# Performance work log

Hardware: AMD Instinct MI355X
Metric: run time of the kernel (lower is better)

Reference implementation:

```python
import jax, jax.numpy as jnp
import numpy as np

SCORE_T = 0.4   # self.score_t
NMS_T = 0.4     # self.nms_t
TOP_K = 200     # nms top_k


def setup_inputs() -> dict:
    key = jax.random.key(0)
    k1, k2, k3, k4, k5 = jax.random.split(key, 5)
    B, S, A, C = 1, 32768, 8, 80
    return {
        "box_pred": jax.random.normal(k1, (B, S, A, 4), jnp.float32),
        "box_conf": jax.random.uniform(k2, (B, S, A, 1), jnp.float32),
        "box_prob": jax.random.uniform(k3, (B, S, A, C), jnp.float32),
        "priors": jax.random.uniform(k4, (B, S, A, 4), jnp.float32),
        "img_shape": jax.random.uniform(k5, (1, 4), jnp.float32),
    }


def _decode(box_pred, box_conf, box_prob, priors, img_shape):
    # box decode: xy += prior xy, wh *= prior wh; then corners
    xy = box_pred[..., 0:2] + priors[..., 0:2]
    wh = box_pred[..., 2:4] * priors[..., 2:4]
    corners = jnp.concatenate([xy - 0.5 * wh, xy + 0.5 * wh], axis=-1)
    # grid normalization: x by 30, y by 10
    corners = corners / jnp.asarray([30.0, 10.0, 30.0, 10.0], corners.dtype)
    # class scores = objectness * class prob, max over classes
    all_scores = box_conf * box_prob                     # [B,S,A,C]
    cls_scores = jnp.max(all_scores, axis=-1)            # [B,S,A]
    cls_ids = jnp.argmax(all_scores, axis=-1)            # [B,S,A]
    valid = cls_scores > SCORE_T
    # flatten candidates; scale to image coords (same math as scaling post-filter)
    boxes = corners.reshape(-1, 4) * img_shape.reshape(1, 4)
    scores = jnp.where(valid.reshape(-1), cls_scores.reshape(-1), -1.0)
    classes = cls_ids.reshape(-1).astype(jnp.int32)
    return boxes, scores, classes


def _greedy_nms_keep(top_boxes, top_scores):
    # padded greedy NMS over the fixed top-K candidates (score-desc order)
    valid = top_scores > SCORE_T  # padded/invalid entries carry score -1
    b = jax.lax.stop_gradient(top_boxes)
    x1, y1, x2, y2 = b[:, 0], b[:, 1], b[:, 2], b[:, 3]
    area = (x2 - x1) * (y2 - y1)
    xx1 = jnp.maximum(x1[:, None], x1[None, :])
    yy1 = jnp.maximum(y1[:, None], y1[None, :])
    xx2 = jnp.minimum(x2[:, None], x2[None, :])
    yy2 = jnp.minimum(y2[:, None], y2[None, :])
    inter = jnp.clip(xx2 - xx1, 0.0) * jnp.clip(yy2 - yy1, 0.0)
    iou = inter / (area[:, None] + area[None, :] - inter)  # [K,K]
    idxs = jnp.arange(TOP_K)

    def body(i, keep):
        # candidate i (highest remaining score), suppress later overlapping boxes
        sup = keep[i] & (iou[i] > NMS_T) & (idxs > i)
        return keep & ~sup

    return jax.lax.fori_loop(0, TOP_K, body, valid)


def reference(box_pred, box_conf, box_prob, priors, img_shape):
    boxes, scores, classes = _decode(box_pred, box_conf, box_prob, priors, img_shape)
    top_scores, top_idx = jax.lax.top_k(scores, TOP_K)
    top_boxes = boxes[top_idx]
    top_classes = classes[top_idx]
    keep = _greedy_nms_keep(top_boxes, top_scores)
    count = jnp.sum(keep).astype(jnp.int32)
    # compact kept detections to the front (score-descending), zero-pad rest
    order = jnp.argsort(jnp.where(keep, 0, 1))  # stable sort keeps score order
    kmask = keep[order]
    out_boxes = jnp.where(kmask[:, None], top_boxes[order], 0.0)
    out_scores = jnp.where(kmask, top_scores[order], 0.0)
    out_classes = jnp.where(kmask, top_classes[order], -1)
    return out_boxes, out_scores, out_classes, count
```

## Files before the change

### kernel.cpp

```cpp
#include <hip/hip_runtime.h>
#include <stdint.h>

typedef unsigned long long u64;

#define N_ANCH (32768 * 8)
#define N_CLS 80
#define TOPK 200
#define CAP 4096
#define NBINS2 4096
#define BASE12 0x3ECCCu
#define POISON 0xAAAAAAAAu
#define SCORE_T 0.4f
#define NMS_T 0.4f


#define OFF_SCORES 0
#define OFF_CLS    (N_ANCH * 4)
#define OFF_HIST   (N_ANCH * 5)
#define OFF_CNT    (OFF_HIST + NBINS2 * 4)
#define OFF_CPK    (OFF_CNT + 16)
#define OFF_CSC    (OFF_CPK + CAP * 4)

#define AGLD(p) __hip_atomic_load((p), __ATOMIC_RELAXED, __HIP_MEMORY_SCOPE_AGENT)
#define AGST(p, v) __hip_atomic_store((p), (v), __ATOMIC_RELAXED, __HIP_MEMORY_SCOPE_AGENT)


__global__ __launch_bounds__(256) void k_score(
    const float* __restrict__ conf, const float* __restrict__ prob,
    float* __restrict__ scores, unsigned char* __restrict__ cls8,
    unsigned* __restrict__ hist) {
  const int l = threadIdx.x;
  const int g = l >> 2, q = l & 3;
  const int a = blockIdx.x * 64 + g;
  const float c = conf[a];
  const float4* p = (const float4*)(prob + (size_t)a * N_CLS + q * 20);
  float best = -1.0f;
  int bcls = 0;
#pragma unroll
  for (int k = 0; k < 5; ++k) {
    const float4 v = p[k];
    const int cb = q * 20 + k * 4;
    const float s0 = c * v.x, s1 = c * v.y, s2 = c * v.z, s3 = c * v.w;
    if (s0 > best) { best = s0; bcls = cb; }
    if (s1 > best) { best = s1; bcls = cb + 1; }
    if (s2 > best) { best = s2; bcls = cb + 2; }
    if (s3 > best) { best = s3; bcls = cb + 3; }
  }
  u64 key = ((u64)__float_as_uint(best) << 32) | (unsigned)(255 - bcls);
  const u64 o1 = __shfl_xor(key, 1, 4); key = key > o1 ? key : o1;
  const u64 o2 = __shfl_xor(key, 2, 4); key = key > o2 ? key : o2;
  if (q == 0) {
    const float s = __uint_as_float((unsigned)(key >> 32));
    const int cls = 255 - (int)(key & 0xFFu);
    const bool valid = s > SCORE_T;
    scores[a] = valid ? s : -1.0f;
    cls8[a] = (unsigned char)cls;
    if (valid) {
      unsigned bin = (__float_as_uint(s) >> 12) - BASE12;
      bin = bin > (NBINS2 - 1u) ? (NBINS2 - 1u) : bin;
      atomicAdd(&hist[bin], 1u);
    }
  }
}

__global__ __launch_bounds__(512) void k_compact_final(
    const float* __restrict__ scores, const unsigned char* __restrict__ cls8,
    uint4* __restrict__ hist4, const float* __restrict__ pred,
    const float* __restrict__ priors, const float* __restrict__ img,
    unsigned* __restrict__ cnt, unsigned* __restrict__ cpk,
    unsigned* __restrict__ cscb, float* __restrict__ out) {
  __shared__ unsigned tsum[256];
  __shared__ unsigned s_thr;
  const int t = threadIdx.x;
  const bool owner = t < 256;

  unsigned h[16];
  if (owner) {
    unsigned tot = 0;
#pragma unroll
    for (int v = 0; v < 4; ++v) {
      const uint4 hv = hist4[t * 4 + v];
      h[v * 4 + 0] = hv.x - POISON; h[v * 4 + 1] = hv.y - POISON;
      h[v * 4 + 2] = hv.z - POISON; h[v * 4 + 3] = hv.w - POISON;
      tot += h[v * 4 + 0] + h[v * 4 + 1] + h[v * 4 + 2] + h[v * 4 + 3];
    }
    tsum[t] = tot;
  }
  __syncthreads();
  for (int d = 1; d < 256; d <<= 1) {
    unsigned v = 0;
    if (owner && t + d < 256) v = tsum[t + d];
    __syncthreads();
    if (owner) tsum[t] += v;
    __syncthreads();
  }
  if (owner) {
    unsigned run = (t < 255) ? tsum[t + 1] : 0u;
#pragma unroll
    for (int k = 15; k >= 0; --k) {
      const unsigned nrun = run + h[k];
      if (nrun >= TOPK && run < TOPK)
        s_thr = ((unsigned)(t * 16 + k) + BASE12) << 12;
      run = nrun;
    }
    if (t == 0 && tsum[0] < TOPK) s_thr = 0u;
  }
  __syncthreads();

  {
    const unsigned lo = s_thr;
    const int i4 = blockIdx.x * 512 + t;
    const float4 s4 = ((const float4*)scores)[i4];
#pragma unroll
    for (int k = 0; k < 4; ++k) {
      const float s = (k == 0) ? s4.x : (k == 1) ? s4.y : (k == 2) ? s4.z : s4.w;
      const int i = i4 * 4 + k;
      if (s > SCORE_T && __float_as_uint(s) >= lo) {
        const unsigned pos = atomicAdd(&cnt[0], 1u) - POISON;
        if (pos < CAP) {
          AGST(&cpk[pos], ((unsigned)i << 8) | (unsigned)cls8[i]);
          AGST(&cscb[pos], __float_as_uint(s));
        }
      }
    }
  }

  __shared__ int s_last;
  asm volatile("s_waitcnt vmcnt(0)" ::: "memory");
  __syncthreads();
  if (t == 0)
    s_last = (atomicAdd(&cnt[2], 1u) == POISON + (unsigned)(gridDim.x - 1));
  __syncthreads();
  if (!s_last) return;

  const unsigned m = AGLD(&cnt[0]) - POISON;

  {
    const uint4 pz = make_uint4(POISON, POISON, POISON, POISON);
    hist4[t] = pz;
    hist4[512 + t] = pz;
    if (t == 0) { cnt[0] = POISON; cnt[2] = POISON; }
  }

  __shared__ u64 kb[CAP];
  __shared__ unsigned ti[TOPK];
  __shared__ float tsc[TOPK];
  __shared__ float tcl[TOPK];
  __shared__ float4 bxv[TOPK];
  __shared__ float ar[TOPK];
  __shared__ u64 adj[TOPK][4];
  __shared__ u64 kw[4];
  __shared__ int s_cnt;

  const int M = (int)(m < (unsigned)CAP ? m : (unsigned)CAP);
  const int Mpad = (M + 7) & ~7;
  const int Kp = M < TOPK ? M : TOPK;

  for (int i = t; i < Mpad; i += 512) {
    kb[i] = (i < M)
                ? (((u64)AGLD(&cscb[i]) << 32) | (unsigned)(~AGLD(&cpk[i])))
                : 0ull;
  }
  if (t < TOPK) {
    bxv[t] = make_float4(0.f, 0.f, 0.f, 0.f);
    ar[t] = 0.f;
  }
  __syncthreads();

  for (int e = t; e < M; e += 512) {
    const u64 ke = kb[e];
    int r = 0;
#pragma unroll 8
    for (int j = 0; j < Mpad; ++j) r += (kb[j] > ke);
    if (r < TOPK) {
      const unsigned cp = ~(unsigned)ke;
      ti[r] = cp >> 8;
      tsc[r] = __uint_as_float((unsigned)(ke >> 32));
      tcl[r] = (float)(cp & 0xFFu);
    }
  }
  __syncthreads();

  if (t < Kp) {
    const unsigned idx = ti[t];
    const float4 pd = ((const float4*)pred)[idx];
    const float4 pr = ((const float4*)priors)[idx];
    const float4 im = *(const float4*)img;
    const float x = pd.x + pr.x, y = pd.y + pr.y;
    const float w = pd.z * pr.z, h = pd.w * pr.w;
    const float x1 = ((x - 0.5f * w) / 30.0f) * im.x;
    const float y1 = ((y - 0.5f * h) / 10.0f) * im.y;
    const float x2 = ((x + 0.5f * w) / 30.0f) * im.z;
    const float y2 = ((y + 0.5f * h) / 10.0f) * im.w;
    bxv[t] = make_float4(x1, y1, x2, y2);
    ar[t] = (x2 - x1) * (y2 - y1);
  }
  __syncthreads();

  {
    const int wv = t >> 6, ln = t & 63;
#pragma unroll 5
    for (int r = 0; r < 25; ++r) {
      const int i = wv + r * 8;
      const float4 bi = bxv[i];
      const float ai = ar[i];
#pragma unroll
      for (int wq = 0; wq < 4; ++wq) {
        const int j = wq * 64 + ln;
        const int jc = j < TOPK ? j : TOPK - 1;
        const float4 bj = bxv[jc];
        const float aj = ar[jc];
        const float xx1 = fmaxf(bi.x, bj.x);
        const float yy1 = fmaxf(bi.y, bj.y);
        const float xx2 = fminf(bi.z, bj.z);
        const float yy2 = fminf(bi.w, bj.w);
        const float inter = fmaxf(xx2 - xx1, 0.0f) * fmaxf(yy2 - yy1, 0.0f);
        const float iou = inter / (ai + aj - inter);
        const bool sup = (iou > NMS_T) & (j > i) & (j < Kp);
        const u64 b = __ballot(sup);
        if (ln == 0) adj[i][wq] = b;
      }
    }
  }
  __syncthreads();

  if (t == 0) {
    auto initw = [&](int w) -> u64 {
      const int lo = w * 64;
      if (Kp <= lo) return 0ull;
      const int n = Kp - lo;
      return n >= 64 ? ~0ull : ((1ull << n) - 1ull);
    };
    u64 k0 = initw(0), k1 = initw(1), k2 = initw(2), k3 = initw(3);
#pragma unroll 8
    for (int i = 0; i < TOPK; ++i) {
      const u64 r0 = adj[i][0], r1 = adj[i][1], r2 = adj[i][2], r3 = adj[i][3];
      const u64 kwv = (i < 64) ? k0 : (i < 128) ? k1 : (i < 192) ? k2 : k3;
      const u64 msk = 0ull - ((kwv >> (i & 63)) & 1ull);
      k0 &= ~(r0 & msk);
      k1 &= ~(r1 & msk);
      k2 &= ~(r2 & msk);
      k3 &= ~(r3 & msk);
    }
    kw[0] = k0; kw[1] = k1; kw[2] = k2; kw[3] = k3;
    s_cnt = __popcll(k0) + __popcll(k1) + __popcll(k2) + __popcll(k3);
  }
  __syncthreads();

  const int count = s_cnt;
  if (t < TOPK) {
    const bool kept = (t < Kp) && ((kw[t >> 6] >> (t & 63)) & 1ull);
    if (kept) {
      int pos = 0;
      for (int w = 0; w < (t >> 6); ++w) pos += __popcll(kw[w]);
      pos += __popcll(kw[t >> 6] & ((1ull << (t & 63)) - 1ull));
      out[pos * 4 + 0] = bxv[t].x;
      out[pos * 4 + 1] = bxv[t].y;
      out[pos * 4 + 2] = bxv[t].z;
      out[pos * 4 + 3] = bxv[t].w;
      out[800 + pos] = tsc[t];
      out[1000 + pos] = tcl[t];
    }
    if (t >= count) {
      out[t * 4 + 0] = 0.0f;
      out[t * 4 + 1] = 0.0f;
      out[t * 4 + 2] = 0.0f;
      out[t * 4 + 3] = 0.0f;
      out[800 + t] = 0.0f;
      out[1000 + t] = -1.0f;
    }
  }
  if (t == 0) out[1200] = (float)count;
}

extern "C" void kernel_launch(void* const* d_in, const int* in_sizes, int n_in,
                              void* d_out, int out_size, void* d_ws,
                              size_t ws_size, hipStream_t stream) {
  const float* pred   = (const float*)d_in[0];
  const float* conf   = (const float*)d_in[1];
  const float* prob   = (const float*)d_in[2];
  const float* priors = (const float*)d_in[3];
  const float* img    = (const float*)d_in[4];
  float* out = (float*)d_out;

  char* ws = (char*)d_ws;
  float* scores        = (float*)(ws + OFF_SCORES);
  unsigned char* cls8  = (unsigned char*)(ws + OFF_CLS);
  unsigned* hist       = (unsigned*)(ws + OFF_HIST);
  unsigned* cnt        = (unsigned*)(ws + OFF_CNT);
  unsigned* cpk        = (unsigned*)(ws + OFF_CPK);
  unsigned* cscb       = (unsigned*)(ws + OFF_CSC);

  k_score<<<N_ANCH / 64, 256, 0, stream>>>(conf, prob, scores, cls8, hist);
  k_compact_final<<<N_ANCH / 2048, 512, 0, stream>>>(
      scores, cls8, (uint4*)hist, pred, priors, img, cnt, cpk, cscb, out);
}
```

Before: 70.59 us.

## Fuse scoring and compaction into one persistent kernel with a grid barrier

Merges the scoring kernel and the compaction/NMS kernel into a single launch of 256 blocks. Each block scores 1024 anchors and keeps the scores and class ids in registers. A spin-wait grid barrier on a counter waits until the histogram is complete, then each block computes the threshold and compacts its own candidates. This removes the global scores and class buffers, their write and re-read traffic, and one kernel launch. In exchange it relies on all 256 blocks being co-resident for the spin barrier, and it has less parallelism in the scoring phase.

```diff
diff --git a/kernel.cpp b/kernel.cpp
--- a/kernel.cpp
+++ b/kernel.cpp
@@ -13,88 +13,95 @@
 #define SCORE_T 0.4f
 #define NMS_T 0.4f
 
-
-#define OFF_SCORES 0
-#define OFF_CLS    (N_ANCH * 4)
-#define OFF_HIST   (N_ANCH * 5)
-#define OFF_CNT    (OFF_HIST + NBINS2 * 4)
-#define OFF_CPK    (OFF_CNT + 16)
-#define OFF_CSC    (OFF_CPK + CAP * 4)
+#define NBLK 256
+#define APB (N_ANCH / NBLK)
+#define PASSES (APB / 128)
+
+
+#define OFF_HIST 0
+#define OFF_CNT  (NBINS2 * 4)
+#define OFF_CPK  (OFF_CNT + 16)
+#define OFF_CSC  (OFF_CPK + CAP * 4)
 
 #define AGLD(p) __hip_atomic_load((p), __ATOMIC_RELAXED, __HIP_MEMORY_SCOPE_AGENT)
 #define AGST(p, v) __hip_atomic_store((p), (v), __ATOMIC_RELAXED, __HIP_MEMORY_SCOPE_AGENT)
 
 
-__global__ __launch_bounds__(256) void k_score(
+__global__ __launch_bounds__(512) void k_fused(
     const float* __restrict__ conf, const float* __restrict__ prob,
-    float* __restrict__ scores, unsigned char* __restrict__ cls8,
-    unsigned* __restrict__ hist) {
-  const int l = threadIdx.x;
-  const int g = l >> 2, q = l & 3;
-  const int a = blockIdx.x * 64 + g;
-  const float c = conf[a];
-  const float4* p = (const float4*)(prob + (size_t)a * N_CLS + q * 20);
-  float best = -1.0f;
-  int bcls = 0;
-#pragma unroll
-  for (int k = 0; k < 5; ++k) {
-    const float4 v = p[k];
-    const int cb = q * 20 + k * 4;
-    const float s0 = c * v.x, s1 = c * v.y, s2 = c * v.z, s3 = c * v.w;
-    if (s0 > best) { best = s0; bcls = cb; }
-    if (s1 > best) { best = s1; bcls = cb + 1; }
-    if (s2 > best) { best = s2; bcls = cb + 2; }
-    if (s3 > best) { best = s3; bcls = cb + 3; }
-  }
-  u64 key = ((u64)__float_as_uint(best) << 32) | (unsigned)(255 - bcls);
-  const u64 o1 = __shfl_xor(key, 1, 4); key = key > o1 ? key : o1;
-  const u64 o2 = __shfl_xor(key, 2, 4); key = key > o2 ? key : o2;
-  if (q == 0) {
-    const float s = __uint_as_float((unsigned)(key >> 32));
-    const int cls = 255 - (int)(key & 0xFFu);
-    const bool valid = s > SCORE_T;
-    scores[a] = valid ? s : -1.0f;
-    cls8[a] = (unsigned char)cls;
-    if (valid) {
-      unsigned bin = (__float_as_uint(s) >> 12) - BASE12;
-      bin = bin > (NBINS2 - 1u) ? (NBINS2 - 1u) : bin;
-      atomicAdd(&hist[bin], 1u);
-    }
-  }
-}
-
-__global__ __launch_bounds__(512) void k_compact_final(
-    const float* __restrict__ scores, const unsigned char* __restrict__ cls8,
-    uint4* __restrict__ hist4, const float* __restrict__ pred,
-    const float* __restrict__ priors, const float* __restrict__ img,
+    const float* __restrict__ pred, const float* __restrict__ priors,
+    const float* __restrict__ img, unsigned* __restrict__ hist,
     unsigned* __restrict__ cnt, unsigned* __restrict__ cpk,
     unsigned* __restrict__ cscb, float* __restrict__ out) {
+  const int t = threadIdx.x;
+  const int g = t >> 2, q = t & 3;
+  const int blk = blockIdx.x;
+
+  float sreg[PASSES];
+  int creg[PASSES];
+#pragma unroll
+  for (int p = 0; p < PASSES; ++p) {
+    const int a = blk * APB + p * 128 + g;
+    const float c = conf[a];
+    const float4* pp = (const float4*)(prob + (size_t)a * N_CLS + q * 20);
+    float best = -1.0f;
+    int bcls = 0;
+#pragma unroll
+    for (int k = 0; k < 5; ++k) {
+      const float4 v = pp[k];
+      const int cb = q * 20 + k * 4;
+      const float s0 = c * v.x, s1 = c * v.y, s2 = c * v.z, s3 = c * v.w;
+      if (s0 > best) { best = s0; bcls = cb; }
+      if (s1 > best) { best = s1; bcls = cb + 1; }
+      if (s2 > best) { best = s2; bcls = cb + 2; }
+      if (s3 > best) { best = s3; bcls = cb + 3; }
+    }
+    u64 key = ((u64)__float_as_uint(best) << 32) | (unsigned)(255 - bcls);
+    const u64 o1 = __shfl_xor(key, 1, 4); key = key > o1 ? key : o1;
+    const u64 o2 = __shfl_xor(key, 2, 4); key = key > o2 ? key : o2;
+    const float s = __uint_as_float((unsigned)(key >> 32));
+    if (q == 0) {
+      const bool valid = s > SCORE_T;
+      sreg[p] = valid ? s : -1.0f;
+      creg[p] = 255 - (int)(key & 0xFFu);
+      if (valid) {
+        unsigned bin = (__float_as_uint(s) >> 12) - BASE12;
+        bin = bin > (NBINS2 - 1u) ? (NBINS2 - 1u) : bin;
+        atomicAdd(&hist[bin], 1u);
+      }
+    }
+  }
+
+  asm volatile("s_waitcnt vmcnt(0)" ::: "memory");
+  __syncthreads();
+  if (t == 0) {
+    atomicAdd(&cnt[2], 1u);
+    while (AGLD(&cnt[2]) != POISON + (unsigned)NBLK)
+      __builtin_amdgcn_s_sleep(2);
+  }
+  __syncthreads();
+
   __shared__ unsigned tsum[256];
   __shared__ unsigned s_thr;
-  const int t = threadIdx.x;
-  const bool owner = t < 256;
-
   unsigned h[16];
-  if (owner) {
+  if (t < 256) {
     unsigned tot = 0;
 #pragma unroll
-    for (int v = 0; v < 4; ++v) {
-      const uint4 hv = hist4[t * 4 + v];
-      h[v * 4 + 0] = hv.x - POISON; h[v * 4 + 1] = hv.y - POISON;
-      h[v * 4 + 2] = hv.z - POISON; h[v * 4 + 3] = hv.w - POISON;
-      tot += h[v * 4 + 0] + h[v * 4 + 1] + h[v * 4 + 2] + h[v * 4 + 3];
+    for (int k = 0; k < 16; ++k) {
+      h[k] = AGLD(&hist[t * 16 + k]) - POISON;
+      tot += h[k];
     }
     tsum[t] = tot;
   }
   __syncthreads();
   for (int d = 1; d < 256; d <<= 1) {
     unsigned v = 0;
-    if (owner && t + d < 256) v = tsum[t + d];
+    if (t < 256 && t + d < 256) v = tsum[t + d];
     __syncthreads();
-    if (owner) tsum[t] += v;
+    if (t < 256) tsum[t] += v;
     __syncthreads();
   }
-  if (owner) {
+  if (t < 256) {
     unsigned run = (t < 255) ? tsum[t + 1] : 0u;
 #pragma unroll
     for (int k = 15; k >= 0; --k) {
@@ -109,17 +116,17 @@
 
   {
     const unsigned lo = s_thr;
-    const int i4 = blockIdx.x * 512 + t;
-    const float4 s4 = ((const float4*)scores)[i4];
-#pragma unroll
-    for (int k = 0; k < 4; ++k) {
-      const float s = (k == 0) ? s4.x : (k == 1) ? s4.y : (k == 2) ? s4.z : s4.w;
-      const int i = i4 * 4 + k;
-      if (s > SCORE_T && __float_as_uint(s) >= lo) {
-        const unsigned pos = atomicAdd(&cnt[0], 1u) - POISON;
-        if (pos < CAP) {
-          AGST(&cpk[pos], ((unsigned)i << 8) | (unsigned)cls8[i]);
-          AGST(&cscb[pos], __float_as_uint(s));
+    if (q == 0) {
+#pragma unroll
+      for (int p = 0; p < PASSES; ++p) {
+        const float s = sreg[p];
+        if (s > SCORE_T && __float_as_uint(s) >= lo) {
+          const unsigned pos = atomicAdd(&cnt[0], 1u) - POISON;
+          if (pos < CAP) {
+            const unsigned a = (unsigned)(blk * APB + p * 128 + g);
+            AGST(&cpk[pos], (a << 8) | (unsigned)creg[p]);
+            AGST(&cscb[pos], __float_as_uint(s));
+          }
         }
       }
     }
@@ -129,17 +136,18 @@
   asm volatile("s_waitcnt vmcnt(0)" ::: "memory");
   __syncthreads();
   if (t == 0)
-    s_last = (atomicAdd(&cnt[2], 1u) == POISON + (unsigned)(gridDim.x - 1));
+    s_last = (atomicAdd(&cnt[3], 1u) == POISON + (unsigned)(NBLK - 1));
   __syncthreads();
   if (!s_last) return;
 
   const unsigned m = AGLD(&cnt[0]) - POISON;
 
   {
+    uint4* h4 = (uint4*)hist;
     const uint4 pz = make_uint4(POISON, POISON, POISON, POISON);
-    hist4[t] = pz;
-    hist4[512 + t] = pz;
-    if (t == 0) { cnt[0] = POISON; cnt[2] = POISON; }
+    h4[t] = pz;
+    h4[512 + t] = pz;
+    if (t == 0) { cnt[0] = POISON; cnt[2] = POISON; cnt[3] = POISON; }
   }
 
   __shared__ u64 kb[CAP];
@@ -187,11 +195,11 @@
     const float4 pr = ((const float4*)priors)[idx];
     const float4 im = *(const float4*)img;
     const float x = pd.x + pr.x, y = pd.y + pr.y;
-    const float w = pd.z * pr.z, h = pd.w * pr.w;
+    const float w = pd.z * pr.z, hh = pd.w * pr.w;
     const float x1 = ((x - 0.5f * w) / 30.0f) * im.x;
-    const float y1 = ((y - 0.5f * h) / 10.0f) * im.y;
+    const float y1 = ((y - 0.5f * hh) / 10.0f) * im.y;
     const float x2 = ((x + 0.5f * w) / 30.0f) * im.z;
-    const float y2 = ((y + 0.5f * h) / 10.0f) * im.w;
+    const float y2 = ((y + 0.5f * hh) / 10.0f) * im.w;
     bxv[t] = make_float4(x1, y1, x2, y2);
     ar[t] = (x2 - x1) * (y2 - y1);
   }
@@ -284,14 +292,11 @@
   float* out = (float*)d_out;
 
   char* ws = (char*)d_ws;
-  float* scores        = (float*)(ws + OFF_SCORES);
-  unsigned char* cls8  = (unsigned char*)(ws + OFF_CLS);
-  unsigned* hist       = (unsigned*)(ws + OFF_HIST);
-  unsigned* cnt        = (unsigned*)(ws + OFF_CNT);
-  unsigned* cpk        = (unsigned*)(ws + OFF_CPK);
-  unsigned* cscb       = (unsigned*)(ws + OFF_CSC);
-
-  k_score<<<N_ANCH / 64, 256, 0, stream>>>(conf, prob, scores, cls8, hist);
-  k_compact_final<<<N_ANCH / 2048, 512, 0, stream>>>(
-      scores, cls8, (uint4*)hist, pred, priors, img, cnt, cpk, cscb, out);
+  unsigned* hist = (unsigned*)(ws + OFF_HIST);
+  unsigned* cnt  = (unsigned*)(ws + OFF_CNT);
+  unsigned* cpk  = (unsigned*)(ws + OFF_CPK);
+  unsigned* cscb = (unsigned*)(ws + OFF_CSC);
+
+  k_fused<<<NBLK, 512, 0, stream>>>(conf, prob, pred, priors, img, hist, cnt,
+                                    cpk, cscb, out);
 }
```

Result: slower. 74.57 us (+5.6%).
